# Kernel tuning notes

Hardware: AMD Instinct MI355X
Metric: run time of the kernel (lower is better)

Reference implementation:

```python
import jax, jax.numpy as jnp
import numpy as np

B, S_V, S_E = 4, 768, 64
S = S_V + S_E
W_V, W_E = 2048, 1024
H, HKV, DH = 8, 1, 256
MLP_V, MLP_E = 16384, 4096
EPS = 1e-6
SCALE = DH ** -0.5


def setup_inputs() -> dict:
    key = jax.random.key(0)
    ks = iter(jax.random.split(key, 40))
    rn = lambda shape, s=0.02: jax.random.normal(next(ks), shape, jnp.float32) * s
    inp = {
        "embeds_vlm": jax.random.normal(next(ks), (B, S_V, W_V), jnp.float32),
        "embeds_exp": jax.random.normal(next(ks), (B, S_E, W_E), jnp.float32),
        "cond": jax.random.normal(next(ks), (B, W_E), jnp.float32),
        "vlm_ln1_w": rn((W_V,)), "vlm_ln2_w": rn((W_V,)),
        "vlm_q_w": rn((W_V, H * DH)), "vlm_k_w": rn((W_V, HKV * DH)), "vlm_v_w": rn((W_V, HKV * DH)),
        "vlm_o_w": rn((H * DH, W_V)),
        "vlm_gate_w": rn((W_V, MLP_V)), "vlm_up_w": rn((W_V, MLP_V)), "vlm_down_w": rn((MLP_V, W_V)),
        "exp_ln1_dw": rn((W_E, 3 * W_E)), "exp_ln1_db": rn((3 * W_E,)),
        "exp_ln2_dw": rn((W_E, 3 * W_E)), "exp_ln2_db": rn((3 * W_E,)),
        "exp_q_w": rn((W_E, H * DH)), "exp_k_w": rn((W_E, HKV * DH)), "exp_v_w": rn((W_E, HKV * DH)),
        "exp_o_w": rn((H * DH, W_E)),
        "exp_gate_w": rn((W_E, MLP_E)), "exp_up_w": rn((W_E, MLP_E)), "exp_down_w": rn((MLP_E, W_E)),
    }
    inp["position_ids"] = jnp.broadcast_to(jnp.arange(S, dtype=jnp.int32), (B, S))
    # additive joint mask: prefix (VLM) fully bidirectional, expert attends
    # to the full prefix and causally within the expert suffix.
    allow = np.zeros((S, S), dtype=bool)
    allow[:S_V, :S_V] = True
    allow[S_V:, :S_V] = True
    allow[S_V:, S_V:] = np.tril(np.ones((S_E, S_E), dtype=bool))
    mask = np.where(allow, 0.0, -1e9).astype(np.float32)
    inp["attn_mask"] = jnp.broadcast_to(jnp.asarray(mask)[None, None], (B, 1, S, S))
    return inp


def _rms(x):
    return x * jax.lax.rsqrt(jnp.mean(x * x, axis=-1, keepdims=True) + EPS)


def _rope(x, pos):
    half = DH // 2
    inv = 1.0 / (10000.0 ** (jnp.arange(0, DH, 2, dtype=jnp.float32) / DH))
    freqs = pos.astype(jnp.float32)[:, :, None] * inv  # [B,S,DH/2]
    emb = jnp.concatenate([freqs, freqs], axis=-1)     # [B,S,DH]
    cos = jnp.cos(emb)[:, None]                        # unsqueeze head dim -> [B,1,S,DH]
    sin = jnp.sin(emb)[:, None]
    x1, x2 = x[..., :half], x[..., half:]
    return x * cos + jnp.concatenate([-x2, x1], axis=-1) * sin


def _heads(x, n):  # [B,S,n*DH] -> [B,n,S,DH]
    return x.reshape(x.shape[0], x.shape[1], n, DH).transpose(0, 2, 1, 3)


def _mlp(x, gw, uw, dw):  # Gemma gated MLP, gelu_pytorch_tanh
    return (jax.nn.gelu(x @ gw, approximate=True) * (x @ uw)) @ dw


def reference(embeds_vlm, embeds_exp, cond, position_ids, attn_mask,
              vlm_ln1_w, vlm_ln2_w, vlm_q_w, vlm_k_w, vlm_v_w, vlm_o_w,
              vlm_gate_w, vlm_up_w, vlm_down_w,
              exp_ln1_dw, exp_ln1_db, exp_ln2_dw, exp_ln2_db,
              exp_q_w, exp_k_w, exp_v_w, exp_o_w,
              exp_gate_w, exp_up_w, exp_down_w):
    # --- pre-attention norms (VLM: plain GemmaRMSNorm; expert: AdaRMSNorm) ---
    hv = _rms(embeds_vlm) * (1.0 + vlm_ln1_w)
    mod1 = cond @ exp_ln1_dw + exp_ln1_db                  # [B, 3*W_E]
    s1, sh1, g1 = jnp.split(mod1[:, None, :], 3, axis=-1)  # each [B,1,W_E]
    he = _rms(embeds_exp) * (1.0 + s1) + sh1

    # --- per-model qkv projections, joint concat over sequence ---
    q = jnp.concatenate([_heads(hv @ vlm_q_w, H), _heads(he @ exp_q_w, H)], axis=2)      # [B,H,S,DH]
    k = jnp.concatenate([_heads(hv @ vlm_k_w, HKV), _heads(he @ exp_k_w, HKV)], axis=2)  # [B,1,S,DH]
    v = jnp.concatenate([_heads(hv @ vlm_v_w, HKV), _heads(he @ exp_v_w, HKV)], axis=2)

    q = _rope(q, position_ids)
    k = _rope(k, position_ids)
    k = jnp.broadcast_to(k, (B, H, S, DH))  # repeat_kv (n_rep = H // HKV)
    v = jnp.broadcast_to(v, (B, H, S, DH))

    logits = jnp.einsum('bhqd,bhkd->bhqk', q, k) * SCALE + attn_mask
    probs = jax.nn.softmax(logits.astype(jnp.float32), axis=-1).astype(q.dtype)
    attn = jnp.einsum('bhqk,bhkd->bhqd', probs, v)
    attn = attn.transpose(0, 2, 1, 3).reshape(B, S, H * DH)

    av, ae = attn[:, :S_V], attn[:, S_V:]
    hv1 = embeds_vlm + av @ vlm_o_w               # gate None for VLM
    he1 = embeds_exp + (ae @ exp_o_w) * g1        # gated residual for expert

    # --- post-attention norm + MLP ---
    nv = _rms(hv1) * (1.0 + vlm_ln2_w)
    mod2 = cond @ exp_ln2_dw + exp_ln2_db
    s2, sh2, g2 = jnp.split(mod2[:, None, :], 3, axis=-1)
    ne = _rms(he1) * (1.0 + s2) + sh2

    out_v = hv1 + _mlp(nv, vlm_gate_w, vlm_up_w, vlm_down_w)
    out_e = he1 + _mlp(ne, exp_gate_w, exp_up_w, exp_down_w) * g2
    return (out_v, out_e)
```

## Files before the change

kernel.cpp:

```cpp
#include <hip/hip_runtime.h>
#include <math.h>

#define BATCH 4
#define S_V 768
#define S_E 64
#define SEQ 832
#define W_V 2048
#define W_E 1024
#define NH 8
#define DH 256
#define MLP_V 16384
#define MLP_E 4096
#define EPS 1e-6f
#define ATT_SCALE 0.0625f
#define LOG2E 1.4426950408889634f

typedef __attribute__((ext_vector_type(8))) __bf16 bf16x8;
typedef __attribute__((ext_vector_type(4))) float f32x4;

__device__ __forceinline__ short f2bf(float f) {
    union { float f; unsigned u; } v; v.f = f;
    unsigned r = v.u + 0x7FFFu + ((v.u >> 16) & 1u);
    return (short)(r >> 16);
}
__device__ __forceinline__ float bf2f(short s) {
    union { unsigned u; float f; } v;
    v.u = ((unsigned)(unsigned short)s) << 16;
    return v.f;
}

#define G2L(gp, lp)                                                          \
    __builtin_amdgcn_global_load_lds(                                        \
        (const __attribute__((address_space(1))) unsigned int*)              \
            (unsigned long long)(const void*)(gp),                           \
        (__attribute__((address_space(3))) unsigned int*)                    \
            (unsigned int)(unsigned long long)(const void*)(lp),             \
        16, 0, 0)

__global__ __launch_bounds__(256) void bgemm_k(
    const short* __restrict__ A, const short* __restrict__ Bt,
    float* __restrict__ C, short* __restrict__ Cb,
    const float* __restrict__ res, const float* __restrict__ gate, int gate_off,
    int N, int K, int rpb,
    long long a_bs, long long c_bs, long long r_bs, int flags)
{
    __shared__ short Asd[4096];
    __shared__ short Bsd[4096];

    const int t  = threadIdx.x;
    const int bm = blockIdx.y * 128;
    const int bn = blockIdx.x * 128;

    const short* gA[2];
    const short* gB[2];
    int lof[2];
#pragma unroll
    for (int l = 0; l < 2; l++) {
        int off = l * 4096 + t * 16;
        int row = off >> 6;
        int kel = (off & 63) >> 1;
        lof[l] = off;
        int m = bm + row;
        gA[l] = A + (long long)(m / rpb) * a_bs + (long long)(m % rpb) * K + kel;
        gB[l] = Bt + (long long)(bn + row) * K + kel;
    }

    const int lane = t & 63;
    const int w    = t >> 6;
    const int wm   = (w >> 1) * 64;
    const int wn   = (w & 1) * 64;
    const int lr   = lane & 15;
    const int quad = lane >> 4;

    f32x4 acc[4][4];
#pragma unroll
    for (int i = 0; i < 4; i++)
#pragma unroll
        for (int j = 0; j < 4; j++) acc[i][j] = (f32x4){0.f, 0.f, 0.f, 0.f};

    for (int k0 = 0; k0 < K; k0 += 32) {
        __syncthreads();
#pragma unroll
        for (int l = 0; l < 2; l++) {
            G2L(gA[l] + k0, (char*)Asd + lof[l]);
            G2L(gB[l] + k0, (char*)Bsd + lof[l]);
        }
        __syncthreads();

        bf16x8 af[4], bfr[4];
#pragma unroll
        for (int i = 0; i < 4; i++)
            af[i] = *(const bf16x8*)&Asd[(wm + i * 16 + lr) * 32 + quad * 8];
#pragma unroll
        for (int j = 0; j < 4; j++)
            bfr[j] = *(const bf16x8*)&Bsd[(wn + j * 16 + lr) * 32 + quad * 8];
#pragma unroll
        for (int i = 0; i < 4; i++)
#pragma unroll
            for (int j = 0; j < 4; j++)
                acc[i][j] = __builtin_amdgcn_mfma_f32_16x16x32_bf16(
                    af[i], bfr[j], acc[i][j], 0, 0, 0);
    }

#pragma unroll
    for (int i = 0; i < 4; i++) {
#pragma unroll
        for (int r = 0; r < 4; r++) {
            int m = bm + wm + i * 16 + quad * 4 + r;
            long long bb = m / rpb;
            long long ss = m % rpb;
            long long rowb = bb * c_bs + ss * (long long)N;
            const float* rp = (flags & 1) ? res + bb * r_bs + ss * (long long)N : nullptr;
            const float* gp = (flags & 2) ? gate + bb * 3072 + gate_off : nullptr;
#pragma unroll
            for (int j = 0; j < 4; j++) {
                int n = bn + wn + j * 16 + lr;
                float v = acc[i][j][r];
                if (flags & 2) v *= gp[n];
                if (flags & 4) v += C[rowb + n];
                if (flags & 1) v += rp[n];
                if (flags & 8) Cb[rowb + n] = f2bf(v);
                else           C[rowb + n] = v;
            }
        }
    }
}

__global__ __launch_bounds__(256) void tcvt_k(
    const float* __restrict__ W, short* __restrict__ Wt, int K, int N)
{
    __shared__ float tile[64][65];
    const int bx = blockIdx.x;
    const int by = blockIdx.y;
    const int t = threadIdx.x;
#pragma unroll
    for (int p = 0; p < 4; p++) {
        int idx = p * 256 + t;
        int r = idx >> 4;
        int c4 = (idx & 15) << 2;
        float4 v = *(const float4*)&W[(long long)(by * 64 + r) * N + bx * 64 + c4];
        tile[r][c4] = v.x; tile[r][c4 + 1] = v.y;
        tile[r][c4 + 2] = v.z; tile[r][c4 + 3] = v.w;
    }
    __syncthreads();
#pragma unroll
    for (int p = 0; p < 8; p++) {
        int idx = p * 256 + t;
        int n  = idx >> 5;
        int kp = idx & 31;
        unsigned lo = (unsigned)(unsigned short)f2bf(tile[kp * 2][n]);
        unsigned hi = (unsigned)(unsigned short)f2bf(tile[kp * 2 + 1][n]);
        *(unsigned*)&Wt[(long long)(bx * 64 + n) * K + by * 64 + kp * 2] =
            lo | (hi << 16);
    }
}

__global__ __launch_bounds__(256) void rms_scale_bf(
    const float* __restrict__ x, const float* __restrict__ w,
    short* __restrict__ out, int C)
{
    const int row = blockIdx.x;
    const int t = threadIdx.x;
    const float* xp = x + (long long)row * C;
    short* op = out + (long long)row * C;
    float ss = 0.f;
    for (int i = t; i < C; i += 256) { float v = xp[i]; ss += v * v; }
    __shared__ float sred[256];
    sred[t] = ss;
    __syncthreads();
    for (int off = 128; off > 0; off >>= 1) {
        if (t < off) sred[t] += sred[t + off];
        __syncthreads();
    }
    float scale = rsqrtf(sred[0] / (float)C + EPS);
    for (int i = t; i < C; i += 256) op[i] = f2bf(xp[i] * scale * (1.f + w[i]));
}

__global__ __launch_bounds__(256) void rms_mod_bf(
    const float* __restrict__ x, const float* __restrict__ mod,
    short* __restrict__ out, int C, int rows_per_b)
{
    const int row = blockIdx.x;
    const int t = threadIdx.x;
    const int b = row / rows_per_b;
    const float* xp = x + (long long)row * C;
    const float* mp = mod + (long long)b * 3072;
    short* op = out + (long long)row * C;
    float ss = 0.f;
    for (int i = t; i < C; i += 256) { float v = xp[i]; ss += v * v; }
    __shared__ float sred[256];
    sred[t] = ss;
    __syncthreads();
    for (int off = 128; off > 0; off >>= 1) {
        if (t < off) sred[t] += sred[t + off];
        __syncthreads();
    }
    float scale = rsqrtf(sred[0] / (float)C + EPS);
    for (int i = t; i < C; i += 256)
        op[i] = f2bf(xp[i] * scale * (1.f + mp[i]) + mp[C + i]);
}

__global__ __launch_bounds__(256) void modln_k(
    const float* __restrict__ cond, const float* __restrict__ dw,
    const float* __restrict__ db, float* __restrict__ out)
{
    const int b = blockIdx.y;
    const int n = blockIdx.x * 256 + threadIdx.x;
    __shared__ float cs[1024];
    for (int i = threadIdx.x; i < 1024; i += 256) cs[i] = cond[b * 1024 + i];
    __syncthreads();
    float acc = db[n];
    for (int k = 0; k < 1024; k++) acc += cs[k] * dw[(long long)k * 3072 + n];
    out[b * 3072 + n] = acc;
}

__global__ __launch_bounds__(128) void rope_bf_k(
    const float* __restrict__ x, short* __restrict__ out,
    const int* __restrict__ pos_ids, int heads, float scale)
{
    const int bs = blockIdx.x;
    const int h = blockIdx.y;
    const int d = threadIdx.x;
    const float p = (float)pos_ids[bs];
    const float inv = powf(10000.f, -(float)d / 128.f);
    const float fr = p * inv;
    const float c = cosf(fr), sn = sinf(fr);
    const float* xp = x + ((long long)bs * heads + h) * DH;
    short* op = out + ((long long)bs * heads + h) * DH;
    float x1 = xp[d];
    float x2 = xp[d + 128];
    op[d]       = f2bf((x1 * c - x2 * sn) * scale);
    op[d + 128] = f2bf((x2 * c + x1 * sn) * scale);
}

__global__ __launch_bounds__(256) void vt_k(
    const short* __restrict__ V, short* __restrict__ Vt)
{
    __shared__ short tile[64][72];
    const int s0 = blockIdx.x * 64;
    const int d0 = blockIdx.y * 64;
    const int b  = blockIdx.z;
    const int t = threadIdx.x;
#pragma unroll
    for (int i = 0; i < 2; i++) {
        int lin = i * 256 + t;
        int r = lin >> 3;
        int c8 = (lin & 7) * 8;
        *(uint4*)&tile[r][c8] =
            *(const uint4*)&V[((long long)(b * SEQ + s0 + r) << 8) + d0 + c8];
    }
    __syncthreads();
#pragma unroll
    for (int i = 0; i < 8; i++) {
        int lin = i * 256 + t;
        int dr = lin >> 5;
        int sp = (lin & 31) * 2;
        unsigned lo = (unsigned)(unsigned short)tile[sp][dr];
        unsigned hi = (unsigned)(unsigned short)tile[sp + 1][dr];
        *(unsigned*)&Vt[(long long)(b * 256 + d0 + dr) * SEQ + s0 + sp] =
            lo | (hi << 16);
    }
}

__global__ __launch_bounds__(256) void attn_mfma_k(
    const short* __restrict__ Qb, const short* __restrict__ Kb,
    const short* __restrict__ Vt, short* __restrict__ out)
{
    __shared__ short Pl[4][16][72];
    const int bx = blockIdx.x;
    const int h  = blockIdx.y;
    const int b  = blockIdx.z;
    const int t  = threadIdx.x;
    const int w    = t >> 6;
    const int lane = t & 63;
    const int lr   = lane & 15;
    const int q4   = lane >> 4;

    const int r0 = bx * 64 + w * 16;
    const int nt = (bx == 12) ? 13 : 12;

    bf16x8 qf[8];
    const short* qrow = Qb + (((long long)(b * SEQ + r0 + lr) * NH + h) << 8) + q4 * 8;
#pragma unroll
    for (int ks = 0; ks < 8; ks++)
        qf[ks] = *(const bf16x8*)(qrow + ks * 32);

    f32x4 acc_o[16];
#pragma unroll
    for (int n = 0; n < 16; n++) acc_o[n] = (f32x4){0.f, 0.f, 0.f, 0.f};
    float m_run[4], l_run[4];
#pragma unroll
    for (int r = 0; r < 4; r++) { m_run[r] = -1e30f; l_run[r] = 0.f; }

    for (int kt = 0; kt < nt; kt++) {
        const int k0 = kt * 64;
        f32x4 s[4];
#pragma unroll
        for (int n = 0; n < 4; n++) {
            s[n] = (f32x4){0.f, 0.f, 0.f, 0.f};
            const short* krow =
                Kb + ((long long)(b * SEQ + k0 + n * 16 + lr) << 8) + q4 * 8;
#pragma unroll
            for (int ks = 0; ks < 8; ks++) {
                bf16x8 kf = *(const bf16x8*)(krow + ks * 32);
                s[n] = __builtin_amdgcn_mfma_f32_16x16x32_bf16(qf[ks], kf, s[n], 0, 0, 0);
            }
        }
        if (bx == 12 && kt == 12) {
#pragma unroll
            for (int n = 0; n < 4; n++) {
                int kg = k0 + n * 16 + lr;
#pragma unroll
                for (int r = 0; r < 4; r++) {
                    int rg = r0 + q4 * 4 + r;
                    if (kg > rg) s[n][r] = -1e30f;
                }
            }
        }
        float mt[4];
#pragma unroll
        for (int r = 0; r < 4; r++)
            mt[r] = fmaxf(fmaxf(s[0][r], s[1][r]), fmaxf(s[2][r], s[3][r]));
#pragma unroll
        for (int off = 8; off >= 1; off >>= 1)
#pragma unroll
            for (int r = 0; r < 4; r++)
                mt[r] = fmaxf(mt[r], __shfl_xor(mt[r], off));
        bool grow = (mt[0] > m_run[0]) | (mt[1] > m_run[1]) |
                    (mt[2] > m_run[2]) | (mt[3] > m_run[3]);
        if (__ballot(grow)) {
            float sf[4];
#pragma unroll
            for (int r = 0; r < 4; r++) {
                float mn = fmaxf(m_run[r], mt[r]);
                sf[r] = exp2f(m_run[r] - mn);
                m_run[r] = mn;
                l_run[r] *= sf[r];
            }
#pragma unroll
            for (int n = 0; n < 16; n++)
#pragma unroll
                for (int r = 0; r < 4; r++) acc_o[n][r] *= sf[r];
        }
        float ts[4] = {0.f, 0.f, 0.f, 0.f};
#pragma unroll
        for (int n = 0; n < 4; n++) {
#pragma unroll
            for (int r = 0; r < 4; r++) {
                float p = exp2f(s[n][r] - m_run[r]);
                ts[r] += p;
                Pl[w][q4 * 4 + r][n * 16 + lr] = f2bf(p);
            }
        }
#pragma unroll
        for (int off = 8; off >= 1; off >>= 1)
#pragma unroll
            for (int r = 0; r < 4; r++) ts[r] += __shfl_xor(ts[r], off);
#pragma unroll
        for (int r = 0; r < 4; r++) l_run[r] += ts[r];
        bf16x8 pa[2];
#pragma unroll
        for (int ss2 = 0; ss2 < 2; ss2++)
            pa[ss2] = *(const bf16x8*)&Pl[w][lr][ss2 * 32 + q4 * 8];
        const short* vbase = Vt + ((long long)b * 256 + lr) * SEQ + k0 + q4 * 8;
#pragma unroll
        for (int n = 0; n < 16; n++) {
            const short* vrow = vbase + (long long)n * 16 * SEQ;
            bf16x8 vf0 = *(const bf16x8*)(vrow);
            bf16x8 vf1 = *(const bf16x8*)(vrow + 32);
            acc_o[n] = __builtin_amdgcn_mfma_f32_16x16x32_bf16(pa[0], vf0, acc_o[n], 0, 0, 0);
            acc_o[n] = __builtin_amdgcn_mfma_f32_16x16x32_bf16(pa[1], vf1, acc_o[n], 0, 0, 0);
        }
    }
    float rinv[4];
#pragma unroll
    for (int r = 0; r < 4; r++) rinv[r] = 1.f / l_run[r];
#pragma unroll
    for (int n = 0; n < 16; n++) {
#pragma unroll
        for (int r = 0; r < 4; r++) {
            int srow = r0 + q4 * 4 + r;
            out[(((long long)(b * SEQ + srow) * NH + h) << 8) + n * 16 + lr] =
                f2bf(acc_o[n][r] * rinv[r]);
        }
    }
}

__global__ __launch_bounds__(256) void gelu_mul_bf(
    short* __restrict__ g, const short* __restrict__ u, long long n4)
{
    long long i = (long long)blockIdx.x * 256 + threadIdx.x;
    if (i >= n4) return;
    uint2 gv = ((const uint2*)g)[i];
    uint2 uv = ((const uint2*)u)[i];
    unsigned w[2] = {gv.x, gv.y};
    unsigned ww[2] = {uv.x, uv.y};
    unsigned o[2];
#pragma unroll
    for (int p = 0; p < 2; p++) {
        unsigned res = 0;
#pragma unroll
        for (int h = 0; h < 2; h++) {
            float x = bf2f((short)((w[p] >> (16 * h)) & 0xFFFF));
            float uu = bf2f((short)((ww[p] >> (16 * h)) & 0xFFFF));
            float th = tanhf(0.7978845608028654f * (x + 0.044715f * x * x * x));
            float r = 0.5f * x * (1.f + th) * uu;
            res |= ((unsigned)(unsigned short)f2bf(r)) << (16 * h);
        }
        o[p] = res;
    }
    ((uint2*)g)[i] = make_uint2(o[0], o[1]);
}

extern "C" void kernel_launch(void* const* d_in, const int* in_sizes, int n_in,
                              void* d_out, int out_size, void* d_ws, size_t ws_size,
                              hipStream_t stream)
{
    const float* embeds_vlm = (const float*)d_in[0];
    const float* embeds_exp = (const float*)d_in[1];
    const float* cond       = (const float*)d_in[2];
    const float* vlm_ln1_w  = (const float*)d_in[3];
    const float* vlm_ln2_w  = (const float*)d_in[4];
    const float* vlm_q_w    = (const float*)d_in[5];
    const float* vlm_k_w    = (const float*)d_in[6];
    const float* vlm_v_w    = (const float*)d_in[7];
    const float* vlm_o_w    = (const float*)d_in[8];
    const float* vlm_gate_w = (const float*)d_in[9];
    const float* vlm_up_w   = (const float*)d_in[10];
    const float* vlm_down_w = (const float*)d_in[11];
    const float* exp_ln1_dw = (const float*)d_in[12];
    const float* exp_ln1_db = (const float*)d_in[13];
    const float* exp_ln2_dw = (const float*)d_in[14];
    const float* exp_ln2_db = (const float*)d_in[15];
    const float* exp_q_w    = (const float*)d_in[16];
    const float* exp_k_w    = (const float*)d_in[17];
    const float* exp_v_w    = (const float*)d_in[18];
    const float* exp_o_w    = (const float*)d_in[19];
    const float* exp_gate_w = (const float*)d_in[20];
    const float* exp_up_w   = (const float*)d_in[21];
    const float* exp_down_w = (const float*)d_in[22];
    const int*   position_ids = (const int*)d_in[23];

    float* OUTV = (float*)d_out;
    float* OUTE = OUTV + (long long)BATCH * S_V * W_V;

    char* p = (char*)d_ws;
    auto alloc = [&](size_t bytes) {
        char* r = p; p += (bytes + 255) & ~(size_t)255; return r;
    };
    short* WT_VQ = (short*)alloc(2048ULL * 2048 * 2);
    short* WT_VK = (short*)alloc(256ULL  * 2048 * 2);
    short* WT_VV = (short*)alloc(256ULL  * 2048 * 2);
    short* WT_VO = (short*)alloc(2048ULL * 2048 * 2);
    short* WT_VG = (short*)alloc(16384ULL * 2048 * 2);
    short* WT_VU = (short*)alloc(16384ULL * 2048 * 2);
    short* WT_VD = (short*)alloc(2048ULL * 16384 * 2);
    short* WT_EQ = (short*)alloc(2048ULL * 1024 * 2);
    short* WT_EK = (short*)alloc(256ULL  * 1024 * 2);
    short* WT_EV = (short*)alloc(256ULL  * 1024 * 2);
    short* WT_EO = (short*)alloc(1024ULL * 2048 * 2);
    short* WT_EG = (short*)alloc(4096ULL * 1024 * 2);
    short* WT_EU = (short*)alloc(4096ULL * 1024 * 2);
    short* WT_ED = (short*)alloc(1024ULL * 4096 * 2);
    short* W0h = (short*)alloc(3072ULL * 2048 * 2);
    short* W1h = (short*)alloc(256ULL * 1024 * 2);
    float* MOD1 = (float*)alloc(4ULL * 3072 * 4);
    float* MOD2 = (float*)alloc(4ULL * 3072 * 4);
    float* Q  = (float*)alloc(4ULL * 832 * 2048 * 4);
    float* Kb = (float*)alloc(4ULL * 832 * 256 * 4);
    short* QBq  = (short*)alloc(4ULL * 832 * 2048 * 2);
    short* KB16 = (short*)alloc(4ULL * 832 * 256 * 2);
    short* VB16 = (short*)alloc(4ULL * 832 * 256 * 2);
    short* VT   = (short*)alloc(4ULL * 256 * 832 * 2);
    short* QB = (short*)alloc(4ULL * 832 * 2048 * 2);
    size_t fixed = (size_t)(p - (char*)d_ws);
    int CR = 3072;
    if (fixed + 2ULL * 3072 * 16384 * 2 + 1024 > ws_size) CR = 768;
    short* G = (short*)alloc((size_t)CR * MLP_V * 2);
    short* U = (short*)alloc((size_t)CR * MLP_V * 2);

    const long long QBS = (long long)SEQ * 2048;
    const long long KBS = (long long)SEQ * 256;

    tcvt_k<<<dim3(2048/64, 2048/64), 256, 0, stream>>>(vlm_q_w, WT_VQ, 2048, 2048);
    tcvt_k<<<dim3(256/64,  2048/64), 256, 0, stream>>>(vlm_k_w, WT_VK, 2048, 256);
    tcvt_k<<<dim3(256/64,  2048/64), 256, 0, stream>>>(vlm_v_w, WT_VV, 2048, 256);
    tcvt_k<<<dim3(2048/64, 2048/64), 256, 0, stream>>>(vlm_o_w, WT_VO, 2048, 2048);
    tcvt_k<<<dim3(16384/64,2048/64), 256, 0, stream>>>(vlm_gate_w, WT_VG, 2048, 16384);
    tcvt_k<<<dim3(16384/64,2048/64), 256, 0, stream>>>(vlm_up_w,   WT_VU, 2048, 16384);
    tcvt_k<<<dim3(2048/64,16384/64), 256, 0, stream>>>(vlm_down_w, WT_VD, 16384, 2048);
    tcvt_k<<<dim3(2048/64, 1024/64), 256, 0, stream>>>(exp_q_w, WT_EQ, 1024, 2048);
    tcvt_k<<<dim3(256/64,  1024/64), 256, 0, stream>>>(exp_k_w, WT_EK, 1024, 256);
    tcvt_k<<<dim3(256/64,  1024/64), 256, 0, stream>>>(exp_v_w, WT_EV, 1024, 256);
    tcvt_k<<<dim3(1024/64, 2048/64), 256, 0, stream>>>(exp_o_w, WT_EO, 2048, 1024);
    tcvt_k<<<dim3(4096/64, 1024/64), 256, 0, stream>>>(exp_gate_w, WT_EG, 1024, 4096);
    tcvt_k<<<dim3(4096/64, 1024/64), 256, 0, stream>>>(exp_up_w,   WT_EU, 1024, 4096);
    tcvt_k<<<dim3(1024/64, 4096/64), 256, 0, stream>>>(exp_down_w, WT_ED, 4096, 1024);

    rms_scale_bf<<<BATCH * S_V, 256, 0, stream>>>(embeds_vlm, vlm_ln1_w, W0h, W_V);
    modln_k<<<dim3(12, BATCH), 256, 0, stream>>>(cond, exp_ln1_dw, exp_ln1_db, MOD1);
    modln_k<<<dim3(12, BATCH), 256, 0, stream>>>(cond, exp_ln2_dw, exp_ln2_db, MOD2);
    rms_mod_bf<<<BATCH * S_E, 256, 0, stream>>>(embeds_exp, MOD1, W1h, W_E, S_E);

    bgemm_k<<<dim3(16, 24), 256, 0, stream>>>(W0h, WT_VQ, Q, nullptr, nullptr, nullptr, 0,
        2048, 2048, S_V, (long long)S_V * 2048, QBS, 0, 0);
    bgemm_k<<<dim3(2, 24), 256, 0, stream>>>(W0h, WT_VK, Kb, nullptr, nullptr, nullptr, 0,
        256, 2048, S_V, (long long)S_V * 2048, KBS, 0, 0);
    bgemm_k<<<dim3(2, 24), 256, 0, stream>>>(W0h, WT_VV, nullptr, VB16, nullptr, nullptr, 0,
        256, 2048, S_V, (long long)S_V * 2048, KBS, 0, 8);
    bgemm_k<<<dim3(16, 2), 256, 0, stream>>>(W1h, WT_EQ, Q + (long long)S_V * 2048,
        nullptr, nullptr, nullptr, 0, 2048, 1024, S_E, (long long)S_E * 1024, QBS, 0, 0);
    bgemm_k<<<dim3(2, 2), 256, 0, stream>>>(W1h, WT_EK, Kb + (long long)S_V * 256,
        nullptr, nullptr, nullptr, 0, 256, 1024, S_E, (long long)S_E * 1024, KBS, 0, 0);
    bgemm_k<<<dim3(2, 2), 256, 0, stream>>>(W1h, WT_EV, nullptr, VB16 + (long long)S_V * 256,
        nullptr, nullptr, 0, 256, 1024, S_E, (long long)S_E * 1024, KBS, 0, 8);

    rope_bf_k<<<dim3(BATCH * SEQ, NH), 128, 0, stream>>>(
        Q, QBq, position_ids, NH, ATT_SCALE * LOG2E);
    rope_bf_k<<<dim3(BATCH * SEQ, 1), 128, 0, stream>>>(
        Kb, KB16, position_ids, 1, 1.0f);
    vt_k<<<dim3(13, 4, BATCH), 256, 0, stream>>>(VB16, VT);
    attn_mfma_k<<<dim3(13, NH, BATCH), 256, 0, stream>>>(QBq, KB16, VT, QB);

    bgemm_k<<<dim3(16, 24), 256, 0, stream>>>(QB, WT_VO, OUTV, nullptr,
        embeds_vlm, nullptr, 0, 2048, 2048, S_V, QBS,
        (long long)S_V * 2048, (long long)S_V * 2048, 1);
    bgemm_k<<<dim3(8, 2), 256, 0, stream>>>(QB + (long long)S_V * 2048, WT_EO, OUTE,
        nullptr, embeds_exp, MOD1, 2048, 1024, 2048, S_E, QBS,
        (long long)S_E * 1024, (long long)S_E * 1024, 1 | 2);

    rms_scale_bf<<<BATCH * S_V, 256, 0, stream>>>(OUTV, vlm_ln2_w, W0h, W_V);
    rms_mod_bf<<<BATCH * S_E, 256, 0, stream>>>(OUTE, MOD2, W1h, W_E, S_E);

    for (int c0 = 0; c0 < 3072; c0 += CR) {
        const short* Ac = W0h + (long long)c0 * 2048;
        long long g4 = (long long)CR * MLP_V / 4;
        bgemm_k<<<dim3(MLP_V / 128, CR / 128), 256, 0, stream>>>(Ac, WT_VG,
            nullptr, G, nullptr, nullptr, 0, MLP_V, 2048, CR,
            (long long)CR * 2048, (long long)CR * MLP_V, 0, 8);
        bgemm_k<<<dim3(MLP_V / 128, CR / 128), 256, 0, stream>>>(Ac, WT_VU,
            nullptr, U, nullptr, nullptr, 0, MLP_V, 2048, CR,
            (long long)CR * 2048, (long long)CR * MLP_V, 0, 8);
        gelu_mul_bf<<<(int)((g4 + 255) / 256), 256, 0, stream>>>(G, U, g4);
        bgemm_k<<<dim3(2048 / 128, CR / 128), 256, 0, stream>>>(G, WT_VD,
            OUTV + (long long)c0 * 2048, nullptr, nullptr, nullptr, 0,
            2048, MLP_V, CR, (long long)CR * MLP_V, (long long)CR * 2048, 0, 4);
    }

    bgemm_k<<<dim3(MLP_E / 128, 2), 256, 0, stream>>>(W1h, WT_EG,
        nullptr, G, nullptr, nullptr, 0, MLP_E, 1024, S_E,
        (long long)S_E * 1024, (long long)S_E * MLP_E, 0, 8);
    bgemm_k<<<dim3(MLP_E / 128, 2), 256, 0, stream>>>(W1h, WT_EU,
        nullptr, U, nullptr, nullptr, 0, MLP_E, 1024, S_E,
        (long long)S_E * 1024, (long long)S_E * MLP_E, 0, 8);
    long long e4 = (long long)256 * MLP_E / 4;
    gelu_mul_bf<<<(int)((e4 + 255) / 256), 256, 0, stream>>>(G, U, e4);
    bgemm_k<<<dim3(1024 / 128, 2), 256, 0, stream>>>(G, WT_ED, OUTE, nullptr,
        nullptr, MOD2, 2048, 1024, MLP_E, S_E,
        (long long)S_E * MLP_E, (long long)S_E * 1024, 0, 4 | 2);
}
```

Measured before the change: 2.639 ms.

## Pipeline GEMM loads through a 4-stage LDS ring with swizzle and XCD remap

Replaces the single-buffered GEMM main loop with a 4-deep LDS ring buffer. Tiles are prefetched three iterations ahead using direct global-to-LDS loads, with explicit vmcnt waits and barriers, so memory latency overlaps the MFMA work. It also XOR-swizzles the LDS layout to reduce bank conflicts and remaps workgroup IDs so neighbouring tiles are grouped per XCD for better L2 reuse. LDS use rises to 64KB per block, which may lower occupancy, and the hand-written waitcnt logic is fragile if the compiler reorders or adds memory operations.

```diff
diff --git a/kernel.cpp b/kernel.cpp
--- a/kernel.cpp
+++ b/kernel.cpp
@@ -44,25 +44,35 @@
     int N, int K, int rpb,
     long long a_bs, long long c_bs, long long r_bs, int flags)
 {
-    __shared__ short Asd[4096];
-    __shared__ short Bsd[4096];
-
-    const int t  = threadIdx.x;
-    const int bm = blockIdx.y * 128;
-    const int bn = blockIdx.x * 128;
-
-    const short* gA[2];
-    const short* gB[2];
-    int lof[2];
-#pragma unroll
-    for (int l = 0; l < 2; l++) {
-        int off = l * 4096 + t * 16;
-        int row = off >> 6;
-        int kel = (off & 63) >> 1;
-        lof[l] = off;
-        int m = bm + row;
-        gA[l] = A + (long long)(m / rpb) * a_bs + (long long)(m % rpb) * K + kel;
-        gB[l] = Bt + (long long)(bn + row) * K + kel;
+    __shared__ short ring[4 * 8192];
+
+    const int t = threadIdx.x;
+
+    const int gx = gridDim.x;
+    const int nwg = gx * gridDim.y;
+    const int orig = blockIdx.y * gx + blockIdx.x;
+    const int qq = nwg >> 3, rr = nwg & 7;
+    const int xcd = orig & 7, oi = orig >> 3;
+    const int wg = (xcd < rr ? xcd * (qq + 1) : rr * (qq + 1) + (xcd - rr) * qq) + oi;
+    const int bm = (wg / gx) * 128;
+    const int bn = (wg % gx) * 128;
+
+    const short* gsrc[4];
+    int ldsb[4];
+#pragma unroll
+    for (int l = 0; l < 4; l++) {
+        int o   = (l & 1) * 4096 + t * 16;
+        int row = o >> 6;
+        int g   = (o >> 4) & 3;
+        int kel = ((g ^ (row & 3)) << 3);
+        if (l < 2) {
+            int m = bm + row;
+            gsrc[l] = A + (long long)(m / rpb) * a_bs + (long long)(m % rpb) * K + kel;
+            ldsb[l] = o;
+        } else {
+            gsrc[l] = Bt + (long long)(bn + row) * K + kel;
+            ldsb[l] = 8192 + o;
+        }
     }
 
     const int lane = t & 63;
@@ -71,6 +81,13 @@
     const int wn   = (w & 1) * 64;
     const int lr   = lane & 15;
     const int quad = lane >> 4;
+    const int swq  = (quad ^ (lr & 3)) << 3;
+
+    int aidx[4], bidx[4];
+#pragma unroll
+    for (int i = 0; i < 4; i++) aidx[i] = (wm + i * 16 + lr) * 32 + swq;
+#pragma unroll
+    for (int j = 0; j < 4; j++) bidx[j] = 4096 + (wn + j * 16 + lr) * 32 + swq;
 
     f32x4 acc[4][4];
 #pragma unroll
@@ -78,28 +95,50 @@
 #pragma unroll
         for (int j = 0; j < 4; j++) acc[i][j] = (f32x4){0.f, 0.f, 0.f, 0.f};
 
-    for (int k0 = 0; k0 < K; k0 += 32) {
-        __syncthreads();
-#pragma unroll
-        for (int l = 0; l < 2; l++) {
-            G2L(gA[l] + k0, (char*)Asd + lof[l]);
-            G2L(gB[l] + k0, (char*)Bsd + lof[l]);
-        }
-        __syncthreads();
-
+    const int NT = K >> 5;
+
+#pragma unroll
+    for (int tt = 0; tt < 3; tt++) {
+        if (tt < NT) {
+#pragma unroll
+            for (int l = 0; l < 4; l++) {
+                G2L(gsrc[l], (char*)ring + tt * 16384 + ldsb[l]);
+                gsrc[l] += 32;
+            }
+        }
+    }
+
+    for (int kt = 0; kt < NT; kt++) {
+        if (kt + 3 < NT) {
+            int b = (kt + 3) & 3;
+#pragma unroll
+            for (int l = 0; l < 4; l++) {
+                G2L(gsrc[l], (char*)ring + b * 16384 + ldsb[l]);
+                gsrc[l] += 32;
+            }
+            asm volatile("s_waitcnt vmcnt(12)" ::: "memory");
+        } else {
+            int rem = NT - 1 - kt;
+            if (rem >= 2)      asm volatile("s_waitcnt vmcnt(8)" ::: "memory");
+            else if (rem == 1) asm volatile("s_waitcnt vmcnt(4)" ::: "memory");
+            else               asm volatile("s_waitcnt vmcnt(0)" ::: "memory");
+        }
+        asm volatile("s_barrier" ::: "memory");
+
+        const short* sb = ring + (kt & 3) * 8192;
         bf16x8 af[4], bfr[4];
 #pragma unroll
-        for (int i = 0; i < 4; i++)
-            af[i] = *(const bf16x8*)&Asd[(wm + i * 16 + lr) * 32 + quad * 8];
-#pragma unroll
-        for (int j = 0; j < 4; j++)
-            bfr[j] = *(const bf16x8*)&Bsd[(wn + j * 16 + lr) * 32 + quad * 8];
+        for (int i = 0; i < 4; i++) af[i]  = *(const bf16x8*)&sb[aidx[i]];
+#pragma unroll
+        for (int j = 0; j < 4; j++) bfr[j] = *(const bf16x8*)&sb[bidx[j]];
 #pragma unroll
         for (int i = 0; i < 4; i++)
 #pragma unroll
             for (int j = 0; j < 4; j++)
                 acc[i][j] = __builtin_amdgcn_mfma_f32_16x16x32_bf16(
                     af[i], bfr[j], acc[i][j], 0, 0, 0);
+        asm volatile("s_waitcnt lgkmcnt(0)" ::: "memory");
+        asm volatile("s_barrier" ::: "memory");
     }
 
 #pragma unroll
```

New measurement: 2.262 ms. -14.3%, faster.
